# Kernel tuning notes

Hardware: AMD Instinct MI355X
Metric: run time of the kernel (lower is better)

Reference implementation:

```python
import jax, jax.numpy as jnp
import numpy as np
from jax import lax

B, H, W, C = 2, 96, 96, 96
D_STATE, D_CONV, EXPAND = 16, 3, 2
D_INNER = EXPAND * C            # 192 (VSSBlock inner width)
DM = D_INNER                    # Mamba d_model; Mamba expand=1 -> mamba d_inner == DM
DT_RANK = -(-DM // 16)          # ceil(192/16) = 12


def setup_inputs() -> dict:
    key = jax.random.key(0)
    ks = jax.random.split(key, 12)
    s = lambda k, shp, sc=0.02: jax.random.normal(k, shp, jnp.float32) * sc
    return {
        "x": jax.random.normal(ks[0], (B, H, W, C), jnp.float32),
        "norm_w": jnp.ones((C,), jnp.float32),
        "norm_b": jnp.zeros((C,), jnp.float32),
        "in_proj_w": s(ks[1], (C, 2 * D_INNER)),
        "conv2d_w": s(ks[2], (D_INNER, 1, D_CONV, D_CONV), 0.1),   # depthwise OIHW
        "m_in_proj_w": s(ks[3], (DM, 2 * DM)),
        "m_conv1d_w": s(ks[4], (DM, 1, D_CONV), 0.1),              # depthwise causal OIL
        "m_conv1d_b": jnp.zeros((DM,), jnp.float32),
        "m_x_proj_w": s(ks[5], (DM, DT_RANK + 2 * D_STATE)),
        "m_dt_proj_w": s(ks[6], (DT_RANK, DM), 0.1),
        "m_dt_proj_b": s(ks[7], (DM,), 0.1),
        "m_A_log": jnp.log(jnp.broadcast_to(
            jnp.arange(1, D_STATE + 1, dtype=jnp.float32), (DM, D_STATE))),
        "m_D": jnp.ones((DM,), jnp.float32),
        "m_out_proj_w": s(ks[8], (DM, DM)),
        "out_proj_w": s(ks[9], (D_INNER, C)),
    }


def _layernorm(x, w, b, eps=1e-5):
    mu = x.mean(-1, keepdims=True)
    var = jnp.mean(jnp.square(x - mu), -1, keepdims=True)
    return (x - mu) * lax.rsqrt(var + eps) * w + b


def _selective_scan(u, delta, A, Bm, Cm, Dv):
    # u, delta: (B,L,D); A: (D,N); Bm, Cm: (B,L,N); Dv: (D,)
    dA = jnp.exp(jnp.einsum('bld,dn->bldn', delta, A))           # (B,L,D,N)
    dBu = jnp.einsum('bld,bln->bldn', delta * u, Bm)             # (B,L,D,N)

    def step(h, inp):
        dA_t, dBu_t, C_t = inp
        h = dA_t * h + dBu_t                                      # (B,D,N)
        y = jnp.einsum('bdn,bn->bd', h, C_t)
        return h, y

    h0 = jnp.zeros((u.shape[0], A.shape[0], A.shape[1]), u.dtype)
    xs = (dA.transpose(1, 0, 2, 3), dBu.transpose(1, 0, 2, 3), Cm.transpose(1, 0, 2))
    _, ys = lax.scan(step, h0, xs)
    return ys.transpose(1, 0, 2) + u * Dv                         # (B,L,D)


def _mamba(seq, m_in_proj_w, m_conv1d_w, m_conv1d_b, m_x_proj_w,
           m_dt_proj_w, m_dt_proj_b, m_A_log, m_D, m_out_proj_w):
    # seq: (B,L,DM)
    xm, z = jnp.split(seq @ m_in_proj_w, 2, axis=-1)
    # causal depthwise conv1d over L
    xc = lax.conv_general_dilated(
        jnp.transpose(xm, (0, 2, 1)), m_conv1d_w, (1,), [(D_CONV - 1, 0)],
        feature_group_count=DM, dimension_numbers=('NCH', 'OIH', 'NCH'))
    xm = jax.nn.silu(jnp.transpose(xc + m_conv1d_b[None, :, None], (0, 2, 1)))
    x_dbl = xm @ m_x_proj_w
    dt, Bm, Cm = jnp.split(x_dbl, [DT_RANK, DT_RANK + D_STATE], axis=-1)
    delta = jax.nn.softplus(dt @ m_dt_proj_w + m_dt_proj_b)
    A = -jnp.exp(m_A_log)
    y = _selective_scan(xm, delta, A, Bm, Cm, m_D)
    return (y * jax.nn.silu(z)) @ m_out_proj_w


def reference(x, norm_w, norm_b, in_proj_w, conv2d_w, m_in_proj_w, m_conv1d_w,
              m_conv1d_b, m_x_proj_w, m_dt_proj_w, m_dt_proj_b, m_A_log, m_D,
              m_out_proj_w, out_proj_w):
    Bsz, Hh, Ww, _ = x.shape
    xn = _layernorm(x, norm_w, norm_b)
    x_in, x_gate = jnp.split(xn @ in_proj_w, 2, axis=-1)          # (B,H,W,D_INNER) x2
    # depthwise 3x3 conv, 'same' padding
    xc = lax.conv_general_dilated(
        jnp.transpose(x_in, (0, 3, 1, 2)), conv2d_w, (1, 1), [(1, 1), (1, 1)],
        feature_group_count=D_INNER, dimension_numbers=('NCHW', 'OIHW', 'NCHW'))
    xc = jax.nn.silu(jnp.transpose(xc, (0, 2, 3, 1)))
    seq = xc.reshape(Bsz, Hh * Ww, D_INNER)
    y = _mamba(seq, m_in_proj_w, m_conv1d_w, m_conv1d_b, m_x_proj_w,
               m_dt_proj_w, m_dt_proj_b, m_A_log, m_D, m_out_proj_w)
    y = y.reshape(Bsz, Hh, Ww, D_INNER) * jax.nn.silu(x_gate)
    return x + y @ out_proj_w
```

## Files before the change

### kernel.cpp

```cpp
#include <hip/hip_runtime.h>

#define DEV_INLINE __device__ __forceinline__

constexpr int BATCH = 2;
constexpr int HH = 96, WW = 96, CC = 96;
constexpr int DI = 192;
constexpr int NS = 16;
constexpr int LSEQ = HH * WW;
constexpr int TT = BATCH * LSEQ;
constexpr int CHUNK = 32;
constexpr int NCHUNK = LSEQ / CHUNK;
constexpr int SUP = 24;
constexpr int NSUP = NCHUNK / SUP;
constexpr int QDN = DI * NS;

typedef __attribute__((ext_vector_type(8))) short bf16x8;
typedef __attribute__((ext_vector_type(4))) float f32x4;

DEV_INLINE float silu_f(float x) { return x / (1.f + __expf(-x)); }
DEV_INLINE float softplus_f(float x) {
  return fmaxf(x, 0.f) + log1pf(__expf(-fabsf(x)));
}
DEV_INLINE ushort f2bf(float f) {
  union { float f; unsigned u; } c; c.f = f;
  unsigned u = c.u + 0x7FFF + ((c.u >> 16) & 1);
  return (ushort)(u >> 16);
}
DEV_INLINE float bf2f(ushort u) {
  union { unsigned u; float f; } c; c.u = ((unsigned)u) << 16; return c.f;
}

__global__ __launch_bounds__(256)
void castw_kernel(const float* __restrict__ w0, const float* __restrict__ w1,
                  const float* __restrict__ w2, const float* __restrict__ w3,
                  const float* __restrict__ wx, const float* __restrict__ wdt,
                  ushort* __restrict__ t0, ushort* __restrict__ t1,
                  ushort* __restrict__ t2, ushort* __restrict__ t3,
                  ushort* __restrict__ t4, ushort* __restrict__ t5)
{
  int id = blockIdx.x * 256 + threadIdx.x;
  if (id < 36864) {
    int k = id % 96, n = id / 96;
    t0[id] = f2bf(w0[k * 384 + n]);
  } else if (id < 110592) {
    int j = id - 36864; int k = j % 192, n = j / 192;
    t1[j] = f2bf(w1[k * 384 + n]);
  } else if (id < 147456) {
    int j = id - 110592; int k = j % 192, n = j / 192;
    t2[j] = f2bf(w2[k * 192 + n]);
  } else if (id < 172032) {
    int j = id - 147456; int k = j % 192, n = j / 192;
    t3[j] = (n < 96) ? f2bf(w3[k * 96 + n]) : (ushort)0;
  } else if (id < 181248) {
    int j = id - 172032; int k = j % 192, n = j / 192;
    float v = 0.f;
    if (n < 16) v = wx[k * 44 + 12 + n];
    else if (n < 32) v = wx[k * 44 + 28 + (n - 16)];
    else if (n < 44) v = wx[k * 44 + (n - 32)];
    t4[j] = f2bf(v);
  } else {
    int j = id - 181248; int r = j % 32, d = j / 32;
    t5[j] = (r < 12) ? f2bf(wdt[r * 192 + d]) : (ushort)0;
  }
}

__global__ __launch_bounds__(256)
void ln_kernel(const float* __restrict__ x, const float* __restrict__ w,
               const float* __restrict__ bb, ushort* __restrict__ xn)
{
  int wid = (blockIdx.x * blockDim.x + threadIdx.x) >> 6;
  int lane = threadIdx.x & 63;
  if (wid >= TT) return;
  const float* xr = x + (size_t)wid * CC;
  float v0 = xr[lane];
  float v1 = (lane < 32) ? xr[64 + lane] : 0.f;
  float s = v0 + v1, ss = v0 * v0 + v1 * v1;
#pragma unroll
  for (int off = 32; off >= 1; off >>= 1) {
    s  += __shfl_xor(s, off);
    ss += __shfl_xor(ss, off);
  }
  float mean = s * (1.f / 96.f);
  float var  = ss * (1.f / 96.f) - mean * mean;
  float rstd = rsqrtf(var + 1e-5f);
  ushort* o = xn + (size_t)wid * CC;
  o[lane] = f2bf((v0 - mean) * rstd * w[lane] + bb[lane]);
  if (lane < 32) o[64 + lane] = f2bf((v1 - mean) * rstd * w[64 + lane] + bb[64 + lane]);
}

template<int EPI, int OUTF>
__global__ __launch_bounds__(256)
void mfma_gemm_kernel(const ushort* __restrict__ A, int lda,
                      const ushort* __restrict__ Bt, int ldb,
                      void* __restrict__ Cout, int ldc, int N, int K,
                      const void* __restrict__ aux, int ldaux)
{
  const int tid = threadIdx.x;
  const int wid = tid >> 6, lane = tid & 63;
  const int wm = wid >> 1, wn = wid & 1;
  const int m0 = blockIdx.x * 128 + wm * 64;
  const int n0 = blockIdx.y * 64 + wn * 32;
  const int l16 = lane & 15, quad = lane >> 4;

  f32x4 acc[4][2];
  const f32x4 z4 = {0.f, 0.f, 0.f, 0.f};
#pragma unroll
  for (int i = 0; i < 4; ++i)
#pragma unroll
    for (int j = 0; j < 2; ++j) acc[i][j] = z4;

  for (int k0 = 0; k0 < K; k0 += 32) {
    bf16x8 xf[4], wf[2];
#pragma unroll
    for (int i = 0; i < 4; ++i)
      xf[i] = *(const bf16x8*)(A + (size_t)(m0 + i * 16 + l16) * lda + k0 + quad * 8);
#pragma unroll
    for (int j = 0; j < 2; ++j)
      wf[j] = *(const bf16x8*)(Bt + (size_t)(n0 + j * 16 + l16) * ldb + k0 + quad * 8);
#pragma unroll
    for (int i = 0; i < 4; ++i)
#pragma unroll
      for (int j = 0; j < 2; ++j)
        acc[i][j] = __builtin_amdgcn_mfma_f32_16x16x32_bf16(wf[j], xf[i], acc[i][j], 0, 0, 0);
  }

#pragma unroll
  for (int i = 0; i < 4; ++i) {
    const int token = m0 + i * 16 + l16;
#pragma unroll
    for (int j = 0; j < 2; ++j) {
      const int nb = n0 + j * 16 + quad * 4;
      if (nb >= N) continue;
      float v[4];
#pragma unroll
      for (int r = 0; r < 4; ++r) v[r] = acc[i][j][r];
      if (EPI == 1) {
        const ushort4 g4 = *(const ushort4*)((const ushort*)aux + (size_t)token * ldaux + nb);
        v[0] *= silu_f(bf2f(g4.x)); v[1] *= silu_f(bf2f(g4.y));
        v[2] *= silu_f(bf2f(g4.z)); v[3] *= silu_f(bf2f(g4.w));
      } else if (EPI == 2) {
        const float4 r4 = *(const float4*)((const float*)aux + (size_t)token * ldaux + nb);
        v[0] += r4.x; v[1] += r4.y; v[2] += r4.z; v[3] += r4.w;
      }
      if (OUTF == 0) {
        *(float4*)((float*)Cout + (size_t)token * ldc + nb) =
            make_float4(v[0], v[1], v[2], v[3]);
      } else {
        ushort4 o;
        o.x = f2bf(v[0]); o.y = f2bf(v[1]); o.z = f2bf(v[2]); o.w = f2bf(v[3]);
        *(ushort4*)((ushort*)Cout + (size_t)token * ldc + nb) = o;
      }
    }
  }
}

__global__ __launch_bounds__(256)
void conv2d_silu_kernel(const ushort* __restrict__ xz0, const float* __restrict__ w,
                        ushort* __restrict__ xc)
{
  __shared__ float ws[DI * 9];
  for (int i = threadIdx.x; i < DI * 9; i += 256) ws[i] = w[i];
  __syncthreads();
  int id = blockIdx.x * 256 + threadIdx.x;
  int dq = id % 48;
  int p  = id / 48;
  int j = p % WW;
  int i = (p / WW) % HH;
  int b = p / (WW * HH);
  int d = dq * 4;
  float a0 = 0.f, a1 = 0.f, a2 = 0.f, a3 = 0.f;
#pragma unroll
  for (int ki = 0; ki < 3; ++ki) {
    int ii = i + ki - 1;
    if (ii < 0 || ii >= HH) continue;
#pragma unroll
    for (int kj = 0; kj < 3; ++kj) {
      int jj = j + kj - 1;
      if (jj < 0 || jj >= WW) continue;
      const ushort4 v = *(const ushort4*)(xz0 + ((size_t)((b * HH + ii) * WW + jj)) * 384 + d);
      int wk = ki * 3 + kj;
      a0 = fmaf(bf2f(v.x), ws[(d + 0) * 9 + wk], a0);
      a1 = fmaf(bf2f(v.y), ws[(d + 1) * 9 + wk], a1);
      a2 = fmaf(bf2f(v.z), ws[(d + 2) * 9 + wk], a2);
      a3 = fmaf(bf2f(v.w), ws[(d + 3) * 9 + wk], a3);
    }
  }
  ushort4 o;
  o.x = f2bf(silu_f(a0)); o.y = f2bf(silu_f(a1));
  o.z = f2bf(silu_f(a2)); o.w = f2bf(silu_f(a3));
  *(ushort4*)(xc + (size_t)p * DI + d) = o;
}

__global__ __launch_bounds__(256)
void mamba_prep_kernel(const ushort* __restrict__ xz1, const float* __restrict__ cw,
                       const float* __restrict__ cb, const ushort* __restrict__ Wxt,
                       const ushort* __restrict__ Wdtt, const float* __restrict__ bdt,
                       ushort* __restrict__ xmb_bf, float* __restrict__ xdbl_bc,
                       float* __restrict__ dlt)
{
  __shared__ ushort sxm[64][200];
  __shared__ ushort sdtb[64][40];
  const int tid = threadIdx.x;
  const int t0 = blockIdx.x * 64;
  const int l0 = t0 % LSEQ;

  for (int i = tid; i < 64 * 40 / 2; i += 256) ((unsigned*)sdtb)[i] = 0;

#pragma unroll
  for (int it = 0; it < 12; ++it) {
    int task = tid + it * 256;
    int dq = task % 48, tl = task / 48;
    int d = dq * 4;
    int t = t0 + tl, l = l0 + tl;
    float a0 = cb[d], a1 = cb[d + 1], a2 = cb[d + 2], a3 = cb[d + 3];
#pragma unroll
    for (int k = 0; k < 3; ++k) {
      if (l + k - 2 < 0) continue;
      const ushort4 v = *(const ushort4*)(xz1 + (size_t)(t + k - 2) * 384 + d);
      a0 = fmaf(bf2f(v.x), cw[(d + 0) * 3 + k], a0);
      a1 = fmaf(bf2f(v.y), cw[(d + 1) * 3 + k], a1);
      a2 = fmaf(bf2f(v.z), cw[(d + 2) * 3 + k], a2);
      a3 = fmaf(bf2f(v.w), cw[(d + 3) * 3 + k], a3);
    }
    ushort4 o;
    o.x = f2bf(silu_f(a0)); o.y = f2bf(silu_f(a1));
    o.z = f2bf(silu_f(a2)); o.w = f2bf(silu_f(a3));
    *(ushort4*)&sxm[tl][d] = o;
    *(ushort4*)(xmb_bf + (size_t)t * DI + d) = o;
  }
  __syncthreads();

  const int wid = tid >> 6, lane = tid & 63;
  const int l16 = lane & 15, quad = lane >> 4;
  const int ts = wid * 16;
  const int token = t0 + ts + l16;
  const f32x4 z4 = {0.f, 0.f, 0.f, 0.f};

  f32x4 acc1[3] = {z4, z4, z4};
  for (int k0 = 0; k0 < 192; k0 += 32) {
    bf16x8 xf = *(const bf16x8*)&sxm[ts + l16][k0 + quad * 8];
#pragma unroll
    for (int j = 0; j < 3; ++j) {
      bf16x8 wf = *(const bf16x8*)(Wxt + (size_t)(j * 16 + l16) * 192 + k0 + quad * 8);
      acc1[j] = __builtin_amdgcn_mfma_f32_16x16x32_bf16(wf, xf, acc1[j], 0, 0, 0);
    }
  }
#pragma unroll
  for (int j = 0; j < 2; ++j)
    *(float4*)(xdbl_bc + (size_t)token * 32 + j * 16 + quad * 4) =
        make_float4(acc1[j][0], acc1[j][1], acc1[j][2], acc1[j][3]);
  if (quad < 3) {
    ushort4 o;
    o.x = f2bf(acc1[2][0]); o.y = f2bf(acc1[2][1]);
    o.z = f2bf(acc1[2][2]); o.w = f2bf(acc1[2][3]);
    *(ushort4*)&sdtb[ts + l16][quad * 4] = o;
  }
  __syncthreads();

  bf16x8 dtf = *(const bf16x8*)&sdtb[ts + l16][quad * 8];
  f32x4 acc2[12];
#pragma unroll
  for (int jj = 0; jj < 12; ++jj) {
    bf16x8 wf = *(const bf16x8*)(Wdtt + (size_t)(jj * 16 + l16) * 32 + quad * 8);
    acc2[jj] = __builtin_amdgcn_mfma_f32_16x16x32_bf16(wf, dtf, z4, 0, 0, 0);
  }
#pragma unroll
  for (int jj = 0; jj < 12; ++jj) {
    const int nb = jj * 16 + quad * 4;
    float4 dv;
    dv.x = softplus_f(acc2[jj][0] + bdt[nb + 0]);
    dv.y = softplus_f(acc2[jj][1] + bdt[nb + 1]);
    dv.z = softplus_f(acc2[jj][2] + bdt[nb + 2]);
    dv.w = softplus_f(acc2[jj][3] + bdt[nb + 3]);
    *(float4*)(dlt + (size_t)token * DI + nb) = dv;
  }
}

__global__ __launch_bounds__(192)
void scan1_kernel(const float* __restrict__ dlt, const ushort* __restrict__ xmb,
                  const float* __restrict__ xdbl_bc, const float* __restrict__ Alog,
                  float* __restrict__ P, float* __restrict__ E)
{
  const int d = threadIdx.x;
  const int g = blockIdx.x % NCHUNK;
  const int b = blockIdx.x / NCHUNK;
  const int t0 = b * LSEQ + g * CHUNK;
  float Av[16];
#pragma unroll
  for (int j = 0; j < 16; ++j) Av[j] = -__expf(Alog[d * 16 + j]);
  float e[16];
#pragma unroll
  for (int j = 0; j < 16; ++j) e[j] = 0.f;
  float sdl = 0.f;
#pragma unroll 2
  for (int l = 0; l < CHUNK; ++l) {
    const int t = t0 + l;
    float dl = dlt[(size_t)t * DI + d];
    float u  = bf2f(xmb[(size_t)t * DI + d]);
    const float4 B0 = *(const float4*)(xdbl_bc + (size_t)t * 32 + 0);
    const float4 B1 = *(const float4*)(xdbl_bc + (size_t)t * 32 + 4);
    const float4 B2 = *(const float4*)(xdbl_bc + (size_t)t * 32 + 8);
    const float4 B3 = *(const float4*)(xdbl_bc + (size_t)t * 32 + 12);
    const float Bv[16] = {B0.x, B0.y, B0.z, B0.w, B1.x, B1.y, B1.z, B1.w,
                          B2.x, B2.y, B2.z, B2.w, B3.x, B3.y, B3.z, B3.w};
    float du = dl * u;
    sdl += dl;
#pragma unroll
    for (int j = 0; j < 16; ++j) {
      float a = __expf(dl * Av[j]);
      e[j] = fmaf(a, e[j], du * Bv[j]);
    }
  }
  size_t base = ((size_t)(b * NCHUNK + g)) * QDN + d * 16;
#pragma unroll
  for (int j = 0; j < 16; ++j) {
    P[base + j] = __expf(Av[j] * sdl);
    E[base + j] = e[j];
  }
}

__global__ __launch_bounds__(256)
void scan2a_kernel(const float* __restrict__ P, const float* __restrict__ E,
                   float* __restrict__ SP, float* __restrict__ SE)
{
  int id = blockIdx.x * 256 + threadIdx.x;
  int q = id % QDN;
  int s = (id / QDN) % NSUP;
  int b = id / (QDN * NSUP);
  float cp = 1.f, ce = 0.f;
#pragma unroll 4
  for (int c = 0; c < SUP; ++c) {
    size_t idx = ((size_t)(b * NCHUNK + s * SUP + c)) * QDN + q;
    float p = P[idx], e = E[idx];
    ce = fmaf(p, ce, e);
    cp *= p;
  }
  SP[id] = cp; SE[id] = ce;
}

__global__ __launch_bounds__(256)
void scan2b_kernel(const float* __restrict__ SP, const float* __restrict__ SE,
                   float* __restrict__ Hsup)
{
  int id = blockIdx.x * 256 + threadIdx.x;
  int q = id % QDN;
  int b = id / QDN;
  float carry = 0.f;
#pragma unroll
  for (int s = 0; s < NSUP; ++s) {
    size_t idx = ((size_t)(b * NSUP + s)) * QDN + q;
    Hsup[idx] = carry;
    carry = fmaf(SP[idx], carry, SE[idx]);
  }
}

__global__ __launch_bounds__(256)
void scan2c_kernel(const float* __restrict__ P, const float* __restrict__ E,
                   const float* __restrict__ Hsup, float* __restrict__ Hin)
{
  int id = blockIdx.x * 256 + threadIdx.x;
  int q = id % QDN;
  int s = (id / QDN) % NSUP;
  int b = id / (QDN * NSUP);
  float h = Hsup[id];
#pragma unroll 4
  for (int c = 0; c < SUP; ++c) {
    size_t idx = ((size_t)(b * NCHUNK + s * SUP + c)) * QDN + q;
    Hin[idx] = h;
    h = fmaf(P[idx], h, E[idx]);
  }
}

__global__ __launch_bounds__(192)
void scan3_kernel(const float* __restrict__ dlt, const ushort* __restrict__ xmb,
                  const float* __restrict__ xdbl_bc, const float* __restrict__ Alog,
                  const float* __restrict__ Dv, const ushort* __restrict__ xz1,
                  const float* __restrict__ Hin, ushort* __restrict__ yout)
{
  const int d = threadIdx.x;
  const int g = blockIdx.x % NCHUNK;
  const int b = blockIdx.x / NCHUNK;
  const int t0 = b * LSEQ + g * CHUNK;
  float Av[16];
#pragma unroll
  for (int j = 0; j < 16; ++j) Av[j] = -__expf(Alog[d * 16 + j]);
  const float Dd = Dv[d];
  float h[16];
  {
    size_t hb = ((size_t)(b * NCHUNK + g)) * QDN + d * 16;
#pragma unroll
    for (int j = 0; j < 16; ++j) h[j] = Hin[hb + j];
  }
#pragma unroll 2
  for (int l = 0; l < CHUNK; ++l) {
    const int t = t0 + l;
    float dl = dlt[(size_t)t * DI + d];
    float u  = bf2f(xmb[(size_t)t * DI + d]);
    const float4 B0 = *(const float4*)(xdbl_bc + (size_t)t * 32 + 0);
    const float4 B1 = *(const float4*)(xdbl_bc + (size_t)t * 32 + 4);
    const float4 B2 = *(const float4*)(xdbl_bc + (size_t)t * 32 + 8);
    const float4 B3 = *(const float4*)(xdbl_bc + (size_t)t * 32 + 12);
    const float4 C0 = *(const float4*)(xdbl_bc + (size_t)t * 32 + 16);
    const float4 C1 = *(const float4*)(xdbl_bc + (size_t)t * 32 + 20);
    const float4 C2 = *(const float4*)(xdbl_bc + (size_t)t * 32 + 24);
    const float4 C3 = *(const float4*)(xdbl_bc + (size_t)t * 32 + 28);
    const float Bv[16] = {B0.x, B0.y, B0.z, B0.w, B1.x, B1.y, B1.z, B1.w,
                          B2.x, B2.y, B2.z, B2.w, B3.x, B3.y, B3.z, B3.w};
    const float Cv[16] = {C0.x, C0.y, C0.z, C0.w, C1.x, C1.y, C1.z, C1.w,
                          C2.x, C2.y, C2.z, C2.w, C3.x, C3.y, C3.z, C3.w};
    float du = dl * u;
    float y0 = 0.f, y1 = 0.f, y2 = 0.f, y3 = 0.f;
#pragma unroll
    for (int j = 0; j < 16; ++j) {
      float a = __expf(dl * Av[j]);
      h[j] = fmaf(a, h[j], du * Bv[j]);
      if ((j & 3) == 0) y0 = fmaf(h[j], Cv[j], y0);
      else if ((j & 3) == 1) y1 = fmaf(h[j], Cv[j], y1);
      else if ((j & 3) == 2) y2 = fmaf(h[j], Cv[j], y2);
      else y3 = fmaf(h[j], Cv[j], y3);
    }
    float y = (y0 + y1) + (y2 + y3) + u * Dd;
    float z = bf2f(xz1[(size_t)t * 384 + 192 + d]);
    yout[(size_t)t * DI + d] = f2bf(y * silu_f(z));
  }
}

extern "C" void kernel_launch(void* const* d_in, const int* in_sizes, int n_in,
                              void* d_out, int out_size, void* d_ws, size_t ws_size,
                              hipStream_t stream)
{
  const float* x         = (const float*)d_in[0];
  const float* norm_w    = (const float*)d_in[1];
  const float* norm_b    = (const float*)d_in[2];
  const float* in_proj_w = (const float*)d_in[3];
  const float* conv2d_w  = (const float*)d_in[4];
  const float* m_in_proj = (const float*)d_in[5];
  const float* m_c1d_w   = (const float*)d_in[6];
  const float* m_c1d_b   = (const float*)d_in[7];
  const float* m_x_proj  = (const float*)d_in[8];
  const float* m_dt_w    = (const float*)d_in[9];
  const float* m_dt_b    = (const float*)d_in[10];
  const float* m_A_log   = (const float*)d_in[11];
  const float* m_D       = (const float*)d_in[12];
  const float* m_out_w   = (const float*)d_in[13];
  const float* out_w     = (const float*)d_in[14];
  float* out = (float*)d_out;

  char* wp = (char*)d_ws;
  auto alloc = [&](size_t bytes) {
    char* r = wp; wp += (bytes + 255) & ~(size_t)255; return r;
  };
  ushort* Wt0    = (ushort*)alloc(36864 * 2);
  ushort* Wt1    = (ushort*)alloc(73728 * 2);
  ushort* Wt2    = (ushort*)alloc(36864 * 2);
  ushort* Wt3    = (ushort*)alloc(24576 * 2);
  ushort* Wxt    = (ushort*)alloc(9216 * 2);
  ushort* Wdtt   = (ushort*)alloc(6144 * 2);
  ushort* xn_bf  = (ushort*)alloc((size_t)TT * 96 * 2);
  ushort* xz0    = (ushort*)alloc((size_t)TT * 384 * 2);
  ushort* xc_bf  = (ushort*)alloc((size_t)TT * 192 * 2);
  ushort* xz1    = (ushort*)alloc((size_t)TT * 384 * 2);
  ushort* xmb_bf = (ushort*)alloc((size_t)TT * 192 * 2);
  float*  xdbl_bc= (float*)alloc((size_t)TT * 32 * 4);
  float*  dlt    = (float*)alloc((size_t)TT * 192 * 4);
  float*  Pb     = (float*)alloc((size_t)BATCH * NCHUNK * QDN * 4);
  float*  Eb     = (float*)alloc((size_t)BATCH * NCHUNK * QDN * 4);
  float*  Hin    = (float*)alloc((size_t)BATCH * NCHUNK * QDN * 4);
  float*  SPb    = (float*)alloc((size_t)BATCH * NSUP * QDN * 4);
  float*  SEb    = (float*)alloc((size_t)BATCH * NSUP * QDN * 4);
  float*  Hsup   = (float*)alloc((size_t)BATCH * NSUP * QDN * 4);
  ushort* yfin   = (ushort*)alloc((size_t)TT * 192 * 2);
  ushort* yg     = (ushort*)alloc((size_t)TT * 192 * 2);

  castw_kernel<<<732, 256, 0, stream>>>(in_proj_w, m_in_proj, m_out_w, out_w,
                                        m_x_proj, m_dt_w,
                                        Wt0, Wt1, Wt2, Wt3, Wxt, Wdtt);
  ln_kernel<<<TT / 4, 256, 0, stream>>>(x, norm_w, norm_b, xn_bf);
  mfma_gemm_kernel<0, 1><<<dim3(TT / 128, 6), 256, 0, stream>>>(
      xn_bf, 96, Wt0, 96, xz0, 384, 384, 96, nullptr, 0);
  conv2d_silu_kernel<<<TT * 48 / 256, 256, 0, stream>>>(xz0, conv2d_w, xc_bf);
  mfma_gemm_kernel<0, 1><<<dim3(TT / 128, 6), 256, 0, stream>>>(
      xc_bf, 192, Wt1, 192, xz1, 384, 384, 192, nullptr, 0);
  mamba_prep_kernel<<<TT / 64, 256, 0, stream>>>(
      xz1, m_c1d_w, m_c1d_b, Wxt, Wdtt, m_dt_b, xmb_bf, xdbl_bc, dlt);
  scan1_kernel<<<BATCH * NCHUNK, 192, 0, stream>>>(dlt, xmb_bf, xdbl_bc, m_A_log, Pb, Eb);
  scan2a_kernel<<<BATCH * NSUP * QDN / 256, 256, 0, stream>>>(Pb, Eb, SPb, SEb);
  scan2b_kernel<<<BATCH * QDN / 256, 256, 0, stream>>>(SPb, SEb, Hsup);
  scan2c_kernel<<<BATCH * NSUP * QDN / 256, 256, 0, stream>>>(Pb, Eb, Hsup, Hin);
  scan3_kernel<<<BATCH * NCHUNK, 192, 0, stream>>>(dlt, xmb_bf, xdbl_bc, m_A_log, m_D, xz1, Hin, yfin);
  mfma_gemm_kernel<1, 1><<<dim3(TT / 128, 3), 256, 0, stream>>>(
      yfin, 192, Wt2, 192, yg, 192, 192, 192, xz0 + 192, 384);
  mfma_gemm_kernel<2, 0><<<dim3(TT / 128, 2), 256, 0, stream>>>(
      yg, 192, Wt3, 192, out, 96, 96, 192, x, 96);
}
```

Baseline: 267.6 us.

## Split fused mamba prep kernel into conv1d, x_proj and dt_proj kernels

Replaces the single mamba_prep kernel, which ran the causal conv1d, x_proj MFMA and dt_proj MFMA with shared-memory staging, with three separate kernels that communicate through global memory. A new padded bf16 buffer carries dt between x_proj and dt_proj. The intent is more parallelism per stage, with one wave per 16-token tile and output column group, and lower register and LDS pressure per kernel. In exchange it adds two kernel launches and extra global round trips for xmb and dt.

```diff
diff --git a/kernel.cpp b/kernel.cpp
--- a/kernel.cpp
+++ b/kernel.cpp
@@ -192,86 +192,84 @@
 }
 
 __global__ __launch_bounds__(256)
-void mamba_prep_kernel(const ushort* __restrict__ xz1, const float* __restrict__ cw,
-                       const float* __restrict__ cb, const ushort* __restrict__ Wxt,
-                       const ushort* __restrict__ Wdtt, const float* __restrict__ bdt,
-                       ushort* __restrict__ xmb_bf, float* __restrict__ xdbl_bc,
-                       float* __restrict__ dlt)
-{
-  __shared__ ushort sxm[64][200];
-  __shared__ ushort sdtb[64][40];
-  const int tid = threadIdx.x;
-  const int t0 = blockIdx.x * 64;
-  const int l0 = t0 % LSEQ;
-
-  for (int i = tid; i < 64 * 40 / 2; i += 256) ((unsigned*)sdtb)[i] = 0;
-
-#pragma unroll
-  for (int it = 0; it < 12; ++it) {
-    int task = tid + it * 256;
-    int dq = task % 48, tl = task / 48;
-    int d = dq * 4;
-    int t = t0 + tl, l = l0 + tl;
-    float a0 = cb[d], a1 = cb[d + 1], a2 = cb[d + 2], a3 = cb[d + 3];
-#pragma unroll
-    for (int k = 0; k < 3; ++k) {
-      if (l + k - 2 < 0) continue;
-      const ushort4 v = *(const ushort4*)(xz1 + (size_t)(t + k - 2) * 384 + d);
-      a0 = fmaf(bf2f(v.x), cw[(d + 0) * 3 + k], a0);
-      a1 = fmaf(bf2f(v.y), cw[(d + 1) * 3 + k], a1);
-      a2 = fmaf(bf2f(v.z), cw[(d + 2) * 3 + k], a2);
-      a3 = fmaf(bf2f(v.w), cw[(d + 3) * 3 + k], a3);
-    }
+void conv1d_silu_kernel(const ushort* __restrict__ xz1, const float* __restrict__ w,
+                        const float* __restrict__ bias, ushort* __restrict__ xm)
+{
+  int id = blockIdx.x * 256 + threadIdx.x;
+  int dq = id % 48;
+  int t  = id / 48;
+  int l  = t % LSEQ;
+  int d  = dq * 4;
+  float a0 = bias[d + 0], a1 = bias[d + 1], a2 = bias[d + 2], a3 = bias[d + 3];
+#pragma unroll
+  for (int k = 0; k < 3; ++k) {
+    if (l + k - 2 < 0) continue;
+    const ushort4 v = *(const ushort4*)(xz1 + (size_t)(t + k - 2) * 384 + d);
+    a0 = fmaf(bf2f(v.x), w[(d + 0) * 3 + k], a0);
+    a1 = fmaf(bf2f(v.y), w[(d + 1) * 3 + k], a1);
+    a2 = fmaf(bf2f(v.z), w[(d + 2) * 3 + k], a2);
+    a3 = fmaf(bf2f(v.w), w[(d + 3) * 3 + k], a3);
+  }
+  ushort4 o;
+  o.x = f2bf(silu_f(a0)); o.y = f2bf(silu_f(a1));
+  o.z = f2bf(silu_f(a2)); o.w = f2bf(silu_f(a3));
+  *(ushort4*)(xm + (size_t)t * DI + d) = o;
+}
+
+__global__ __launch_bounds__(256)
+void xproj_kernel(const ushort* __restrict__ xmb, const ushort* __restrict__ Wxt,
+                  float* __restrict__ xdbl_bc, ushort* __restrict__ dtpad)
+{
+  const int w = blockIdx.x * 4 + (threadIdx.x >> 6);
+  const int lane = threadIdx.x & 63;
+  const int s = w / 3, tile = w % 3;
+  const int l16 = lane & 15, quad = lane >> 4;
+  const int token = s * 16 + l16;
+
+  f32x4 acc = {0.f, 0.f, 0.f, 0.f};
+#pragma unroll
+  for (int k0 = 0; k0 < 192; k0 += 32) {
+    bf16x8 xf = *(const bf16x8*)(xmb + (size_t)token * DI + k0 + quad * 8);
+    bf16x8 wf = *(const bf16x8*)(Wxt + (size_t)(tile * 16 + l16) * 192 + k0 + quad * 8);
+    acc = __builtin_amdgcn_mfma_f32_16x16x32_bf16(wf, xf, acc, 0, 0, 0);
+  }
+  if (tile < 2) {
+    *(float4*)(xdbl_bc + (size_t)token * 32 + tile * 16 + quad * 4) =
+        make_float4(acc[0], acc[1], acc[2], acc[3]);
+  } else {
     ushort4 o;
-    o.x = f2bf(silu_f(a0)); o.y = f2bf(silu_f(a1));
-    o.z = f2bf(silu_f(a2)); o.w = f2bf(silu_f(a3));
-    *(ushort4*)&sxm[tl][d] = o;
-    *(ushort4*)(xmb_bf + (size_t)t * DI + d) = o;
-  }
-  __syncthreads();
-
-  const int wid = tid >> 6, lane = tid & 63;
+    o.x = f2bf(acc[0]); o.y = f2bf(acc[1]); o.z = f2bf(acc[2]); o.w = f2bf(acc[3]);
+    *(ushort4*)(dtpad + (size_t)token * 32 + quad * 4) = o;
+    *(ushort4*)(dtpad + (size_t)token * 32 + 16 + quad * 4) = make_ushort4(0, 0, 0, 0);
+  }
+}
+
+__global__ __launch_bounds__(256)
+void dtproj_kernel(const ushort* __restrict__ dtpad, const ushort* __restrict__ Wdtt,
+                   const float* __restrict__ bdt, float* __restrict__ dlt)
+{
+  const int w = blockIdx.x * 4 + (threadIdx.x >> 6);
+  const int lane = threadIdx.x & 63;
+  const int s = w / 3, cg = w % 3;
   const int l16 = lane & 15, quad = lane >> 4;
-  const int ts = wid * 16;
-  const int token = t0 + ts + l16;
+  const int token = s * 16 + l16;
   const f32x4 z4 = {0.f, 0.f, 0.f, 0.f};
 
-  f32x4 acc1[3] = {z4, z4, z4};
-  for (int k0 = 0; k0 < 192; k0 += 32) {
-    bf16x8 xf = *(const bf16x8*)&sxm[ts + l16][k0 + quad * 8];
-#pragma unroll
-    for (int j = 0; j < 3; ++j) {
-      bf16x8 wf = *(const bf16x8*)(Wxt + (size_t)(j * 16 + l16) * 192 + k0 + quad * 8);
-      acc1[j] = __builtin_amdgcn_mfma_f32_16x16x32_bf16(wf, xf, acc1[j], 0, 0, 0);
-    }
-  }
-#pragma unroll
-  for (int j = 0; j < 2; ++j)
-    *(float4*)(xdbl_bc + (size_t)token * 32 + j * 16 + quad * 4) =
-        make_float4(acc1[j][0], acc1[j][1], acc1[j][2], acc1[j][3]);
-  if (quad < 3) {
-    ushort4 o;
-    o.x = f2bf(acc1[2][0]); o.y = f2bf(acc1[2][1]);
-    o.z = f2bf(acc1[2][2]); o.w = f2bf(acc1[2][3]);
-    *(ushort4*)&sdtb[ts + l16][quad * 4] = o;
-  }
-  __syncthreads();
-
-  bf16x8 dtf = *(const bf16x8*)&sdtb[ts + l16][quad * 8];
-  f32x4 acc2[12];
-#pragma unroll
-  for (int jj = 0; jj < 12; ++jj) {
-    bf16x8 wf = *(const bf16x8*)(Wdtt + (size_t)(jj * 16 + l16) * 32 + quad * 8);
-    acc2[jj] = __builtin_amdgcn_mfma_f32_16x16x32_bf16(wf, dtf, z4, 0, 0, 0);
-  }
-#pragma unroll
-  for (int jj = 0; jj < 12; ++jj) {
-    const int nb = jj * 16 + quad * 4;
+  bf16x8 dtf = *(const bf16x8*)(dtpad + (size_t)token * 32 + quad * 8);
+  f32x4 acc[4];
+#pragma unroll
+  for (int jj = 0; jj < 4; ++jj) {
+    bf16x8 wf = *(const bf16x8*)(Wdtt + (size_t)(cg * 64 + jj * 16 + l16) * 32 + quad * 8);
+    acc[jj] = __builtin_amdgcn_mfma_f32_16x16x32_bf16(wf, dtf, z4, 0, 0, 0);
+  }
+#pragma unroll
+  for (int jj = 0; jj < 4; ++jj) {
+    const int nb = cg * 64 + jj * 16 + quad * 4;
     float4 dv;
-    dv.x = softplus_f(acc2[jj][0] + bdt[nb + 0]);
-    dv.y = softplus_f(acc2[jj][1] + bdt[nb + 1]);
-    dv.z = softplus_f(acc2[jj][2] + bdt[nb + 2]);
-    dv.w = softplus_f(acc2[jj][3] + bdt[nb + 3]);
+    dv.x = softplus_f(acc[jj][0] + bdt[nb + 0]);
+    dv.y = softplus_f(acc[jj][1] + bdt[nb + 1]);
+    dv.z = softplus_f(acc[jj][2] + bdt[nb + 2]);
+    dv.w = softplus_f(acc[jj][3] + bdt[nb + 3]);
     *(float4*)(dlt + (size_t)token * DI + nb) = dv;
   }
 }
@@ -461,6 +459,7 @@
   ushort* xc_bf  = (ushort*)alloc((size_t)TT * 192 * 2);
   ushort* xz1    = (ushort*)alloc((size_t)TT * 384 * 2);
   ushort* xmb_bf = (ushort*)alloc((size_t)TT * 192 * 2);
+  ushort* dtpad  = (ushort*)alloc((size_t)TT * 32 * 2);
   float*  xdbl_bc= (float*)alloc((size_t)TT * 32 * 4);
   float*  dlt    = (float*)alloc((size_t)TT * 192 * 4);
   float*  Pb     = (float*)alloc((size_t)BATCH * NCHUNK * QDN * 4);
@@ -481,8 +480,9 @@
   conv2d_silu_kernel<<<TT * 48 / 256, 256, 0, stream>>>(xz0, conv2d_w, xc_bf);
   mfma_gemm_kernel<0, 1><<<dim3(TT / 128, 6), 256, 0, stream>>>(
       xc_bf, 192, Wt1, 192, xz1, 384, 384, 192, nullptr, 0);
-  mamba_prep_kernel<<<TT / 64, 256, 0, stream>>>(
-      xz1, m_c1d_w, m_c1d_b, Wxt, Wdtt, m_dt_b, xmb_bf, xdbl_bc, dlt);
+  conv1d_silu_kernel<<<TT * 48 / 256, 256, 0, stream>>>(xz1, m_c1d_w, m_c1d_b, xmb_bf);
+  xproj_kernel<<<TT / 16 * 3 / 4, 256, 0, stream>>>(xmb_bf, Wxt, xdbl_bc, dtpad);
+  dtproj_kernel<<<TT / 16 * 3 / 4, 256, 0, stream>>>(dtpad, Wdtt, m_dt_b, dlt);
   scan1_kernel<<<BATCH * NCHUNK, 192, 0, stream>>>(dlt, xmb_bf, xdbl_bc, m_A_log, Pb, Eb);
   scan2a_kernel<<<BATCH * NSUP * QDN / 256, 256, 0, stream>>>(Pb, Eb, SPb, SEb);
   scan2b_kernel<<<BATCH * QDN / 256, 256, 0, stream>>>(SPb, SEb, Hsup);
```

After: 260.3 us. -2.7%, faster.
